# Optimization experiments

Hardware: AMD Instinct MI355X
Metric: run time of the kernel (lower is better)

The kernel has to match this reference:

```python
import jax, jax.numpy as jnp
import numpy as np

NQ = 4  # n_qubits
C64 = jnp.complex64
INV_SQRT2 = np.float32(1.0 / np.sqrt(2.0))
H_GATE = jnp.array([[1.0, 1.0], [1.0, -1.0]], dtype=C64) * INV_SQRT2


def _apply_1q(state, U, q):
    # state: (B, 2,2,2,2) complex; U: (2,2) shared or (B,2,2) per-batch
    s = jnp.moveaxis(state, q + 1, -1)
    if U.ndim == 2:
        s = jnp.einsum('b...i,ji->b...j', s, U)
    else:
        s = jnp.einsum('b...i,bji->b...j', s, U)
    return jnp.moveaxis(s, -1, q + 1)


def _apply_cnot(state, c, t):
    s = jnp.moveaxis(state, (c + 1, t + 1), (-2, -1))
    s = jnp.stack([s[..., 0, :], s[..., 1, ::-1]], axis=-2)  # flip target when control=1
    return jnp.moveaxis(s, (-2, -1), (c + 1, t + 1))


def _ry(theta):
    co = jnp.cos(theta * 0.5).astype(C64)
    si = jnp.sin(theta * 0.5).astype(C64)
    return jnp.stack([jnp.stack([co, -si], -1), jnp.stack([si, co], -1)], -2)


def _rz(theta):
    e = jnp.exp(-0.5j * theta).astype(C64)
    z = jnp.zeros_like(e)
    return jnp.stack([jnp.stack([e, z], -1), jnp.stack([z, jnp.conj(e)], -1)], -2)


def _rx(theta):
    co = jnp.cos(theta * 0.5).astype(C64)
    si = (-1j * jnp.sin(theta * 0.5)).astype(C64)
    return jnp.stack([jnp.stack([co, si], -1), jnp.stack([si, co], -1)], -2)


def _vqc(y, w):
    # y: (B, NQ) float angles-to-encode; w: (n_qlayers, 3, NQ)
    B = y.shape[0]
    state = jnp.zeros((B, 2 ** NQ), C64).at[:, 0].set(1.0).reshape((B,) + (2,) * NQ)
    ry_ang = jnp.arctan(y)
    rz_ang = jnp.arctan(y * y)
    # encoding: H, RY(arctan y), RZ(arctan y^2) on each wire
    for q in range(NQ):
        state = _apply_1q(state, H_GATE, q)
        state = _apply_1q(state, _ry(ry_ang[:, q]), q)
        state = _apply_1q(state, _rz(rz_ang[:, q]), q)
    # ansatz layers: CNOT ring (n_esteps=1), then RX/RY/RZ with weights
    for l in range(w.shape[0]):
        for q in range(NQ):
            state = _apply_cnot(state, q, (q + 1) % NQ)
        for q in range(NQ):
            state = _apply_1q(state, _rx(w[l, 0, q]), q)
            state = _apply_1q(state, _ry(w[l, 1, q]), q)
            state = _apply_1q(state, _rz(w[l, 2, q]), q)
    probs = state.real ** 2 + state.imag ** 2  # (B,2,2,2,2)
    outs = []
    for q in range(NQ):
        p = jnp.moveaxis(probs, q + 1, 1).reshape(B, 2, -1).sum(-1)
        outs.append(p[:, 0] - p[:, 1])  # <Z_q>
    return jnp.stack(outs, -1).astype(y.dtype)


def _qlstm(x, W_in, b_in, W_out, b_out, w_f, w_i, w_u, w_o):
    B = x.shape[0]
    Hdim = W_out.shape[1]
    h0 = jnp.zeros((B, Hdim), x.dtype)
    c0 = jnp.zeros((B, Hdim), x.dtype)

    def step(carry, x_t):
        h, c = carry
        y = jnp.concatenate([h, x_t], axis=1) @ W_in + b_in  # (B, NQ)
        f = jax.nn.sigmoid(_vqc(y, w_f) @ W_out + b_out)
        i = jax.nn.sigmoid(_vqc(y, w_i) @ W_out + b_out)
        g = jnp.tanh(_vqc(y, w_u) @ W_out + b_out)
        o = jax.nn.sigmoid(_vqc(y, w_o) @ W_out + b_out)
        c = f * c + i * g
        h = o * jnp.tanh(c)
        return (h, c), h

    (hT, cT), outs = jax.lax.scan(step, (h0, c0), jnp.swapaxes(x, 0, 1))
    return jnp.swapaxes(outs, 0, 1), hT, cT


def setup_inputs() -> dict:
    key = jax.random.key(0)
    ks = jax.random.split(key, 9)
    B, S, D, Hdim = 512, 256, 64, 128
    x = jax.random.normal(ks[0], (B, S, D), jnp.float32)
    W_in = jax.random.normal(ks[1], (Hdim + D, NQ), jnp.float32) * 0.1
    b_in = jax.random.normal(ks[2], (NQ,), jnp.float32) * 0.1
    W_out = jax.random.normal(ks[3], (NQ, Hdim), jnp.float32) * 0.1
    b_out = jax.random.normal(ks[4], (Hdim,), jnp.float32) * 0.1
    two_pi = np.float32(2.0 * np.pi)
    w_f = jax.random.uniform(ks[5], (1, 3, NQ), jnp.float32, 0.0, two_pi)
    w_i = jax.random.uniform(ks[6], (1, 3, NQ), jnp.float32, 0.0, two_pi)
    w_u = jax.random.uniform(ks[7], (1, 3, NQ), jnp.float32, 0.0, two_pi)
    w_o = jax.random.uniform(ks[8], (1, 3, NQ), jnp.float32, 0.0, two_pi)
    return {'x': x, 'W_in': W_in, 'b_in': b_in, 'W_out': W_out, 'b_out': b_out,
            'w_f': w_f, 'w_i': w_i, 'w_u': w_u, 'w_o': w_o}


def reference(x, W_in, b_in, W_out, b_out, w_f, w_i, w_u, w_o):
    return _qlstm(x, W_in, b_in, W_out, b_out, w_f, w_i, w_u, w_o)
```

## Files before the change

kernel.cpp:

```cpp
#include <hip/hip_runtime.h>
#include <math.h>

#define B_TOT 512
#define S_LEN 256
#define D_IN  64
#define HDIM  128

__device__ __forceinline__ float rcp_f(float x) { return __builtin_amdgcn_rcpf(x); }
__device__ __forceinline__ float rsq_f(float x) { return __builtin_amdgcn_rsqf(x); }
__device__ __forceinline__ float sig_f(float x) { return rcp_f(1.0f + __expf(-x)); }
__device__ __forceinline__ float tanh_f(float x) { return 1.0f - 2.0f * rcp_f(1.0f + __expf(2.0f * x)); }

template<int CTRL>
__device__ __forceinline__ float dpp_add(float v) {
    int t = __builtin_amdgcn_update_dpp(0, __float_as_int(v), CTRL, 0xF, 0xF, true);
    return v + __int_as_float(t);
}

__device__ __forceinline__ float allsum64(float v) {
    v = dpp_add<0xB1>(v);
    v = dpp_add<0x4E>(v);
    v = dpp_add<0x141>(v);
    v = dpp_add<0x140>(v);
    int r0 = __builtin_amdgcn_readlane(__float_as_int(v), 0);
    int r1 = __builtin_amdgcn_readlane(__float_as_int(v), 16);
    int r2 = __builtin_amdgcn_readlane(__float_as_int(v), 32);
    int r3 = __builtin_amdgcn_readlane(__float_as_int(v), 48);
    return (__int_as_float(r0) + __int_as_float(r1))
         + (__int_as_float(r2) + __int_as_float(r3));
}

__global__ void __launch_bounds__(64, 1) qlstm_kernel(
    const float* __restrict__ x,
    const float* __restrict__ Win,
    const float* __restrict__ bin,
    const float* __restrict__ Wout,
    const float* __restrict__ bout,
    const float* __restrict__ wf,
    const float* __restrict__ wi,
    const float* __restrict__ wu,
    const float* __restrict__ wo,
    float* __restrict__ out)
{
    const int b = blockIdx.x;
    const int l = threadIdx.x;

    const float4* W4 = reinterpret_cast<const float4*>(Win);
    const float4 wh0 = W4[l];
    const float4 wh1 = W4[64 + l];
    const float4 wx  = W4[128 + l];
    const float4 bn4 = *reinterpret_cast<const float4*>(bin);
    const float bn0 = bn4.x * 0.015625f, bn1 = bn4.y * 0.015625f,
                bn2 = bn4.z * 0.015625f, bn3 = bn4.w * 0.015625f;

    float Wo0[4], Wo1[4];
#pragma unroll
    for (int q = 0; q < 4; ++q) {
        Wo0[q] = Wout[q * HDIM + l];
        Wo1[q] = Wout[q * HDIM + 64 + l];
    }
    const float bo0 = bout[l];
    const float bo1 = bout[64 + l];

    float U[4][4][3];
    {
        const float* wg[4] = {wf, wi, wu, wo};
#pragma unroll
        for (int g = 0; g < 4; ++g) {
#pragma unroll
            for (int q = 0; q < 4; ++q) {
                float a  = wg[g][q];
                float be = wg[g][4 + q];
                float sa = sinf(a),  ca = cosf(a);
                float sb = sinf(be), cb = cosf(be);
                U[g][q][0] = -sb;
                U[g][q][1] = cb * sa;
                U[g][q][2] = cb * ca;
            }
        }
    }

    float h0 = 0.f, h1 = 0.f, c0 = 0.f, c1 = 0.f;

    const float* xb = x + (size_t)b * (S_LEN * D_IN) + l;
    float* ob = out + (size_t)b * (S_LEN * HDIM) + l;

    auto step = [&](float xval) {
        float xc0 = fmaf(xval, wx.x, bn0);
        float xc1 = fmaf(xval, wx.y, bn1);
        float xc2 = fmaf(xval, wx.z, bn2);
        float xc3 = fmaf(xval, wx.w, bn3);
        float p0 = fmaf(h0, wh0.x, fmaf(h1, wh1.x, xc0));
        float p1 = fmaf(h0, wh0.y, fmaf(h1, wh1.y, xc1));
        float p2 = fmaf(h0, wh0.z, fmaf(h1, wh1.z, xc2));
        float p3 = fmaf(h0, wh0.w, fmaf(h1, wh1.w, xc3));
        float ys[4];
        ys[0] = allsum64(p0);
        ys[1] = allsum64(p1);
        ys[2] = allsum64(p2);
        ys[3] = allsum64(p3);

        float nx[4], ny[4], nz[4];
#pragma unroll
        for (int q = 0; q < 4; ++q) {
            float y   = ys[q];
            float y2s = y * y;
            float r1  = rsq_f(fmaf(y, y, 1.0f));
            float r2  = rsq_f(fmaf(y2s, y2s, 1.0f));
            float xx  = r1 * r2;
            nx[q] = xx;
            ny[q] = y2s * xx;
            nz[q] = -y * r1;
        }

        float nz01 = nz[0] * nz[1];
        float nz23 = nz[2] * nz[3];
        float TX[4], TY[4], TZ[4];
        TX[0] = nx[0] * nx[1];
        TX[1] = nx[1] * nx[2];
        TX[2] = nx[2] * nx[3];
        TX[3] = TX[0] * nx[3];
        TZ[0] = nz[1] * nz23;
        TZ[1] = nz01;
        TZ[2] = nz01 * nz[2];
        TZ[3] = nz01 * nz23;
        TY[0] = (nx[0] * ny[1]) * nz23;
        TY[1] = (nz[0] * ny[1]) * nx[2];
        TY[2] = (nz01 * ny[2]) * nx[3];
        TY[3] = -(ny[0] * ny[1]) * (nz[2] * ny[3]);

        float pre0[4], pre1[4];
#pragma unroll
        for (int g = 0; g < 4; ++g) {
            float s0 = bo0, s1 = bo1;
#pragma unroll
            for (int q = 0; q < 4; ++q) {
                float z = fmaf(U[g][q][0], TX[q],
                          fmaf(U[g][q][1], TY[q],
                               U[g][q][2] * TZ[q]));
                s0 = fmaf(z, Wo0[q], s0);
                s1 = fmaf(z, Wo1[q], s1);
            }
            pre0[g] = s0; pre1[g] = s1;
        }

        float f0 = sig_f(pre0[0]),  f1 = sig_f(pre1[0]);
        float i0 = sig_f(pre0[1]),  i1 = sig_f(pre1[1]);
        float g0 = tanh_f(pre0[2]), g1 = tanh_f(pre1[2]);
        float o0 = sig_f(pre0[3]),  o1 = sig_f(pre1[3]);
        c0 = fmaf(f0, c0, i0 * g0);
        c1 = fmaf(f1, c1, i1 * g1);
        h0 = o0 * tanh_f(c0);
        h1 = o1 * tanh_f(c1);
    };

    float xg[4], xn[4];
#pragma unroll
    for (int j = 0; j < 4; ++j) {
        xg[j] = xb[(size_t)j * D_IN];
        xn[j] = xb[(size_t)(4 + j) * D_IN];
    }

    float ph0[4], ph1[4];

#pragma unroll
    for (int j = 0; j < 4; ++j) {
        step(xg[j]);
        ph0[j] = h0; ph1[j] = h1;
    }

    for (int g = 1; g < S_LEN / 4; ++g) {
        const int tprev = (g - 1) * 4;
        float* op = ob + (size_t)tprev * HDIM;
#pragma unroll
        for (int j = 0; j < 4; ++j) {
            op[(size_t)j * HDIM]      = ph0[j];
            op[(size_t)j * HDIM + 64] = ph1[j];
        }
#pragma unroll
        for (int j = 0; j < 4; ++j) xg[j] = xn[j];
#pragma unroll
        for (int j = 0; j < 4; ++j) {
            int tn = (g + 1) * 4 + j;
            if (tn > S_LEN - 1) tn = S_LEN - 1;
            xn[j] = xb[(size_t)tn * D_IN];
        }
        float nh0[4], nh1[4];
#pragma unroll
        for (int j = 0; j < 4; ++j) {
            step(xg[j]);
            nh0[j] = h0; nh1[j] = h1;
        }
#pragma unroll
        for (int j = 0; j < 4; ++j) { ph0[j] = nh0[j]; ph1[j] = nh1[j]; }
    }

    {
        const int tprev = S_LEN - 4;
        float* op = ob + (size_t)tprev * HDIM;
#pragma unroll
        for (int j = 0; j < 4; ++j) {
            op[(size_t)j * HDIM]      = ph0[j];
            op[(size_t)j * HDIM + 64] = ph1[j];
        }
    }

    float* hT = out + (size_t)B_TOT * S_LEN * HDIM;
    float* cT = hT + (size_t)B_TOT * HDIM;
    hT[(size_t)b * HDIM + l]      = h0;
    hT[(size_t)b * HDIM + 64 + l] = h1;
    cT[(size_t)b * HDIM + l]      = c0;
    cT[(size_t)b * HDIM + 64 + l] = c1;
}

extern "C" void kernel_launch(void* const* d_in, const int* in_sizes, int n_in,
                              void* d_out, int out_size, void* d_ws, size_t ws_size,
                              hipStream_t stream) {
    qlstm_kernel<<<dim3(B_TOT), dim3(64), 0, stream>>>(
        (const float*)d_in[0],
        (const float*)d_in[1],
        (const float*)d_in[2],
        (const float*)d_in[3],
        (const float*)d_in[4],
        (const float*)d_in[5],
        (const float*)d_in[6],
        (const float*)d_in[7],
        (const float*)d_in[8],
        (float*)d_out);
}
```

Before: 229.9 us.

## Split hidden units across two wavefronts with LDS exchange of partial sums

Launches 128 threads per batch row so each thread owns one hidden unit instead of two, halving per-thread serial work on the recurrent step. The 4-way projection reduction now ends with a swizzle and bpermute inside each wave, followed by an LDS exchange and a barrier to combine the two waves' partial sums. This adds a per-timestep cross-wave barrier and LDS round trip on the critical path in exchange for halving per-lane gate math. Output stores move from the batched deferred scheme to a direct store after each step.

```diff
diff --git a/kernel.cpp b/kernel.cpp
--- a/kernel.cpp
+++ b/kernel.cpp
@@ -17,20 +17,19 @@
     return v + __int_as_float(t);
 }
 
-__device__ __forceinline__ float allsum64(float v) {
+__device__ __forceinline__ float allsum64(float v, int idx32) {
     v = dpp_add<0xB1>(v);
     v = dpp_add<0x4E>(v);
     v = dpp_add<0x141>(v);
     v = dpp_add<0x140>(v);
-    int r0 = __builtin_amdgcn_readlane(__float_as_int(v), 0);
-    int r1 = __builtin_amdgcn_readlane(__float_as_int(v), 16);
-    int r2 = __builtin_amdgcn_readlane(__float_as_int(v), 32);
-    int r3 = __builtin_amdgcn_readlane(__float_as_int(v), 48);
-    return (__int_as_float(r0) + __int_as_float(r1))
-         + (__int_as_float(r2) + __int_as_float(r3));
-}
-
-__global__ void __launch_bounds__(64, 1) qlstm_kernel(
+    int s = __builtin_amdgcn_ds_swizzle(__float_as_int(v), 0x401F);
+    v += __int_as_float(s);
+    int t = __builtin_amdgcn_ds_bpermute(idx32, __float_as_int(v));
+    v += __int_as_float(t);
+    return v;
+}
+
+__global__ void __launch_bounds__(128, 1) qlstm_kernel(
     const float* __restrict__ x,
     const float* __restrict__ Win,
     const float* __restrict__ bin,
@@ -42,25 +41,28 @@
     const float* __restrict__ wo,
     float* __restrict__ out)
 {
-    const int b = blockIdx.x;
-    const int l = threadIdx.x;
+    const int b   = blockIdx.x;
+    const int tid = threadIdx.x;
+    const int w   = tid >> 6;
+    const int l   = tid & 63;
+    const int u   = (w << 6) + l;
+    const int idx32 = (l ^ 32) << 2;
+
+    __shared__ float4 xch[2][2];
 
     const float4* W4 = reinterpret_cast<const float4*>(Win);
-    const float4 wh0 = W4[l];
-    const float4 wh1 = W4[64 + l];
-    const float4 wx  = W4[128 + l];
+    const float4 wh = W4[u];
+    float4 wx;
+    if (l < 32) wx = W4[128 + (w << 5) + l];
+    else        wx = make_float4(0.f, 0.f, 0.f, 0.f);
     const float4 bn4 = *reinterpret_cast<const float4*>(bin);
-    const float bn0 = bn4.x * 0.015625f, bn1 = bn4.y * 0.015625f,
-                bn2 = bn4.z * 0.015625f, bn3 = bn4.w * 0.015625f;
-
-    float Wo0[4], Wo1[4];
-#pragma unroll
-    for (int q = 0; q < 4; ++q) {
-        Wo0[q] = Wout[q * HDIM + l];
-        Wo1[q] = Wout[q * HDIM + 64 + l];
-    }
-    const float bo0 = bout[l];
-    const float bo1 = bout[64 + l];
+    const float bn0 = bn4.x * 0.0078125f, bn1 = bn4.y * 0.0078125f,
+                bn2 = bn4.z * 0.0078125f, bn3 = bn4.w * 0.0078125f;
+
+    float Wo[4];
+#pragma unroll
+    for (int q = 0; q < 4; ++q) Wo[q] = Wout[q * HDIM + u];
+    const float bo_u = bout[u];
 
     float U[4][4][3];
     {
@@ -80,143 +82,115 @@
         }
     }
 
-    float h0 = 0.f, h1 = 0.f, c0 = 0.f, c1 = 0.f;
-
-    const float* xb = x + (size_t)b * (S_LEN * D_IN) + l;
-    float* ob = out + (size_t)b * (S_LEN * HDIM) + l;
-
-    auto step = [&](float xval) {
-        float xc0 = fmaf(xval, wx.x, bn0);
-        float xc1 = fmaf(xval, wx.y, bn1);
-        float xc2 = fmaf(xval, wx.z, bn2);
-        float xc3 = fmaf(xval, wx.w, bn3);
-        float p0 = fmaf(h0, wh0.x, fmaf(h1, wh1.x, xc0));
-        float p1 = fmaf(h0, wh0.y, fmaf(h1, wh1.y, xc1));
-        float p2 = fmaf(h0, wh0.z, fmaf(h1, wh1.z, xc2));
-        float p3 = fmaf(h0, wh0.w, fmaf(h1, wh1.w, xc3));
-        float ys[4];
-        ys[0] = allsum64(p0);
-        ys[1] = allsum64(p1);
-        ys[2] = allsum64(p2);
-        ys[3] = allsum64(p3);
-
-        float nx[4], ny[4], nz[4];
-#pragma unroll
-        for (int q = 0; q < 4; ++q) {
-            float y   = ys[q];
-            float y2s = y * y;
-            float r1  = rsq_f(fmaf(y, y, 1.0f));
-            float r2  = rsq_f(fmaf(y2s, y2s, 1.0f));
-            float xx  = r1 * r2;
-            nx[q] = xx;
-            ny[q] = y2s * xx;
-            nz[q] = -y * r1;
+    float h = 0.f, c = 0.f;
+
+    const float* xb = x + (size_t)b * (S_LEN * D_IN) + ((w << 5) + (l & 31));
+    float* ob = out + (size_t)b * (S_LEN * HDIM) + u;
+
+    float xcur[4], xnxt[4];
+#pragma unroll
+    for (int j = 0; j < 4; ++j) {
+        xcur[j] = xb[(size_t)j * D_IN];
+        xnxt[j] = xb[(size_t)(4 + j) * D_IN];
+    }
+
+    for (int t4 = 0; t4 < S_LEN / 4; ++t4) {
+#pragma unroll
+        for (int j = 0; j < 4; ++j) {
+            const int par = j & 1;
+            const float xv = xcur[j];
+
+            float p0 = fmaf(h, wh.x, fmaf(xv, wx.x, bn0));
+            float p1 = fmaf(h, wh.y, fmaf(xv, wx.y, bn1));
+            float p2 = fmaf(h, wh.z, fmaf(xv, wx.z, bn2));
+            float p3 = fmaf(h, wh.w, fmaf(xv, wx.w, bn3));
+            float y0 = allsum64(p0, idx32);
+            float y1 = allsum64(p1, idx32);
+            float y2 = allsum64(p2, idx32);
+            float y3 = allsum64(p3, idx32);
+
+            if (l == 0) xch[w][par] = make_float4(y0, y1, y2, y3);
+            asm volatile("s_waitcnt lgkmcnt(0)" ::: "memory");
+            __builtin_amdgcn_s_barrier();
+            asm volatile("" ::: "memory");
+            const float4 pv = xch[w ^ 1][par];
+            y0 += pv.x; y1 += pv.y; y2 += pv.z; y3 += pv.w;
+
+            const float ys[4] = {y0, y1, y2, y3};
+
+            float nx[4], ny[4], nz[4];
+#pragma unroll
+            for (int q = 0; q < 4; ++q) {
+                float y   = ys[q];
+                float y2s = y * y;
+                float r1  = rsq_f(fmaf(y, y, 1.0f));
+                float r2  = rsq_f(fmaf(y2s, y2s, 1.0f));
+                float xx  = r1 * r2;
+                nx[q] = xx;
+                ny[q] = y2s * xx;
+                nz[q] = -y * r1;
+            }
+
+            float nz01 = nz[0] * nz[1];
+            float nz23 = nz[2] * nz[3];
+            float TX[4], TY[4], TZ[4];
+            TX[0] = nx[0] * nx[1];
+            TX[1] = nx[1] * nx[2];
+            TX[2] = nx[2] * nx[3];
+            TX[3] = TX[0] * nx[3];
+            TZ[0] = nz[1] * nz23;
+            TZ[1] = nz01;
+            TZ[2] = nz01 * nz[2];
+            TZ[3] = nz01 * nz23;
+            TY[0] = (nx[0] * ny[1]) * nz23;
+            TY[1] = (nz[0] * ny[1]) * nx[2];
+            TY[2] = (nz01 * ny[2]) * nx[3];
+            TY[3] = -(ny[0] * ny[1]) * (nz[2] * ny[3]);
+
+            float pre[4];
+#pragma unroll
+            for (int g = 0; g < 4; ++g) {
+                float s = bo_u;
+#pragma unroll
+                for (int q = 0; q < 4; ++q) {
+                    float z = fmaf(U[g][q][0], TX[q],
+                              fmaf(U[g][q][1], TY[q],
+                                   U[g][q][2] * TZ[q]));
+                    s = fmaf(z, Wo[q], s);
+                }
+                pre[g] = s;
+            }
+
+            float fg = sig_f(pre[0]);
+            float ig = sig_f(pre[1]);
+            float gg = tanh_f(pre[2]);
+            float og = sig_f(pre[3]);
+            c = fmaf(fg, c, ig * gg);
+            h = og * tanh_f(c);
+
+            ob[(size_t)(t4 * 4 + j) * HDIM] = h;
         }
-
-        float nz01 = nz[0] * nz[1];
-        float nz23 = nz[2] * nz[3];
-        float TX[4], TY[4], TZ[4];
-        TX[0] = nx[0] * nx[1];
-        TX[1] = nx[1] * nx[2];
-        TX[2] = nx[2] * nx[3];
-        TX[3] = TX[0] * nx[3];
-        TZ[0] = nz[1] * nz23;
-        TZ[1] = nz01;
-        TZ[2] = nz01 * nz[2];
-        TZ[3] = nz01 * nz23;
-        TY[0] = (nx[0] * ny[1]) * nz23;
-        TY[1] = (nz[0] * ny[1]) * nx[2];
-        TY[2] = (nz01 * ny[2]) * nx[3];
-        TY[3] = -(ny[0] * ny[1]) * (nz[2] * ny[3]);
-
-        float pre0[4], pre1[4];
-#pragma unroll
-        for (int g = 0; g < 4; ++g) {
-            float s0 = bo0, s1 = bo1;
-#pragma unroll
-            for (int q = 0; q < 4; ++q) {
-                float z = fmaf(U[g][q][0], TX[q],
-                          fmaf(U[g][q][1], TY[q],
-                               U[g][q][2] * TZ[q]));
-                s0 = fmaf(z, Wo0[q], s0);
-                s1 = fmaf(z, Wo1[q], s1);
-            }
-            pre0[g] = s0; pre1[g] = s1;
-        }
-
-        float f0 = sig_f(pre0[0]),  f1 = sig_f(pre1[0]);
-        float i0 = sig_f(pre0[1]),  i1 = sig_f(pre1[1]);
-        float g0 = tanh_f(pre0[2]), g1 = tanh_f(pre1[2]);
-        float o0 = sig_f(pre0[3]),  o1 = sig_f(pre1[3]);
-        c0 = fmaf(f0, c0, i0 * g0);
-        c1 = fmaf(f1, c1, i1 * g1);
-        h0 = o0 * tanh_f(c0);
-        h1 = o1 * tanh_f(c1);
-    };
-
-    float xg[4], xn[4];
-#pragma unroll
-    for (int j = 0; j < 4; ++j) {
-        xg[j] = xb[(size_t)j * D_IN];
-        xn[j] = xb[(size_t)(4 + j) * D_IN];
-    }
-
-    float ph0[4], ph1[4];
-
-#pragma unroll
-    for (int j = 0; j < 4; ++j) {
-        step(xg[j]);
-        ph0[j] = h0; ph1[j] = h1;
-    }
-
-    for (int g = 1; g < S_LEN / 4; ++g) {
-        const int tprev = (g - 1) * 4;
-        float* op = ob + (size_t)tprev * HDIM;
+#pragma unroll
+        for (int j = 0; j < 4; ++j) xcur[j] = xnxt[j];
+        const int tb = (t4 + 2) * 4;
 #pragma unroll
         for (int j = 0; j < 4; ++j) {
-            op[(size_t)j * HDIM]      = ph0[j];
-            op[(size_t)j * HDIM + 64] = ph1[j];
-        }
-#pragma unroll
-        for (int j = 0; j < 4; ++j) xg[j] = xn[j];
-#pragma unroll
-        for (int j = 0; j < 4; ++j) {
-            int tn = (g + 1) * 4 + j;
+            int tn = tb + j;
             if (tn > S_LEN - 1) tn = S_LEN - 1;
-            xn[j] = xb[(size_t)tn * D_IN];
-        }
-        float nh0[4], nh1[4];
-#pragma unroll
-        for (int j = 0; j < 4; ++j) {
-            step(xg[j]);
-            nh0[j] = h0; nh1[j] = h1;
-        }
-#pragma unroll
-        for (int j = 0; j < 4; ++j) { ph0[j] = nh0[j]; ph1[j] = nh1[j]; }
-    }
-
-    {
-        const int tprev = S_LEN - 4;
-        float* op = ob + (size_t)tprev * HDIM;
-#pragma unroll
-        for (int j = 0; j < 4; ++j) {
-            op[(size_t)j * HDIM]      = ph0[j];
-            op[(size_t)j * HDIM + 64] = ph1[j];
+            xnxt[j] = xb[(size_t)tn * D_IN];
         }
     }
 
     float* hT = out + (size_t)B_TOT * S_LEN * HDIM;
     float* cT = hT + (size_t)B_TOT * HDIM;
-    hT[(size_t)b * HDIM + l]      = h0;
-    hT[(size_t)b * HDIM + 64 + l] = h1;
-    cT[(size_t)b * HDIM + l]      = c0;
-    cT[(size_t)b * HDIM + 64 + l] = c1;
+    hT[(size_t)b * HDIM + u] = h;
+    cT[(size_t)b * HDIM + u] = c;
 }
 
 extern "C" void kernel_launch(void* const* d_in, const int* in_sizes, int n_in,
                               void* d_out, int out_size, void* d_ws, size_t ws_size,
                               hipStream_t stream) {
-    qlstm_kernel<<<dim3(B_TOT), dim3(64), 0, stream>>>(
+    qlstm_kernel<<<dim3(B_TOT), dim3(128), 0, stream>>>(
         (const float*)d_in[0],
         (const float*)d_in[1],
         (const float*)d_in[2],
```

Result: slower. 317.5 us (+38.1%).
